# Kernel optimization log

Hardware: AMD Instinct MI355X
Metric: run time of the kernel (lower is better)

Reference implementation:

```python
import jax, jax.numpy as jnp
import numpy as np
from jax import lax

K_NN = 20          # cfg.nsample
BN_EPS = 1e-5


def fps(xyz, npoint, farthest0):
    """Furthest point sampling. xyz: [B,N,3] -> idx [B,npoint] (int)."""
    B, N, _ = xyz.shape

    def step(carry, _):
        distance, far = carry                                  # [B,N], [B]
        centroid = jnp.take_along_axis(xyz, far[:, None, None], axis=1)  # [B,1,3]
        d = jnp.sum((xyz - centroid) ** 2, axis=-1)            # [B,N]
        distance = jnp.minimum(distance, d)
        new_far = jnp.argmax(distance, axis=-1)
        return (distance, new_far), far

    init = (jnp.full((B, N), 1e10, dtype=xyz.dtype), farthest0)
    (_, _), idxs = lax.scan(step, init, None, length=npoint)   # idxs: [npoint,B]
    return jnp.transpose(idxs)                                 # [B,npoint]


def setup_inputs() -> dict:
    key = jax.random.key(0)
    k1, k2, k3, k4 = jax.random.split(key, 4)
    B, N, C = 4, 8192, 128
    c_in = C * 2 + 6   # mlps[0]*2 + 6 (use_xyz) = 262
    c_out = 256
    xyz = jax.random.normal(k1, (B, N, 3), dtype=jnp.float32)
    feat = jax.random.normal(k2, (B, N, C), dtype=jnp.float32)
    conv_w = jax.random.normal(k3, (c_in, c_out), dtype=jnp.float32) * 0.05  # 1x1 conv
    bn_gamma = jnp.ones((c_out,), dtype=jnp.float32)
    bn_beta = jnp.zeros((c_out,), dtype=jnp.float32)
    init_farthest = jax.random.randint(k4, (B,), 0, N)
    return {"xyz": xyz, "feat": feat, "conv_w": conv_w, "bn_gamma": bn_gamma,
            "bn_beta": bn_beta, "init_farthest": init_farthest, "npoints": 2048}


def reference(xyz, feat, conv_w, bn_gamma, bn_beta, init_farthest, npoints):
    # --- FPS sampling ---
    sample_idx = fps(xyz, npoints, init_farthest)                      # [B,S]
    new_xyz = jnp.take_along_axis(xyz, sample_idx[:, :, None], axis=1)  # [B,S,3]

    # --- augment features with xyz (use_xyz=True) ---
    feat_aug = jnp.concatenate([feat, xyz], axis=-1)                   # [B,N,131]
    new_feat_aug = jnp.take_along_axis(feat_aug, sample_idx[:, :, None], axis=1)  # [B,S,131]

    # --- KNN of new_xyz in xyz (squared L2, ascending) ---
    d2 = (jnp.sum(new_xyz ** 2, -1)[:, :, None]
          - 2.0 * jnp.einsum('bsd,bnd->bsn', new_xyz, xyz)
          + jnp.sum(xyz ** 2, -1)[:, None, :])                         # [B,S,N]
    _, knn_idx = lax.top_k(-d2, K_NN)                                  # [B,S,K]

    # --- gather neighbor features, build edge features ---
    knn_feat = jax.vmap(lambda f, i: f[i])(feat_aug, knn_idx)          # [B,S,K,131]
    center = new_feat_aug[:, :, None, :]                               # [B,S,1,131]
    edge = jnp.concatenate(
        [knn_feat - center, jnp.broadcast_to(center, knn_feat.shape)], axis=-1)  # [B,S,K,262]

    # --- shared MLP: 1x1 conv + BN (batch stats) + ReLU ---
    h = jnp.einsum('bskc,co->bsko', edge, conv_w)                      # [B,S,K,256]
    mean = jnp.mean(h, axis=(0, 1, 2))
    var = jnp.var(h, axis=(0, 1, 2))
    h = (h - mean) * lax.rsqrt(var + BN_EPS) * bn_gamma + bn_beta
    h = jax.nn.relu(h)

    # --- max-pool over K neighbors ---
    new_feat = jnp.max(h, axis=2)                                      # [B,S,256]
    return (new_xyz, new_feat, sample_idx)
```

## Files before the change

### kernel.cpp

```cpp
#include <hip/hip_runtime.h>
#include <hip/hip_bf16.h>


#define NPTS   8192
#define NSAMP  2048
#define KNN    20

typedef unsigned long long u64;
typedef unsigned int u32;
typedef unsigned short u16;

template<int CTRL, int RM>
__device__ __forceinline__ u64 dpp_kmax(u64 k) {
  unsigned lo = (unsigned)k, hi = (unsigned)(k >> 32);
  unsigned lo2 = (unsigned)__builtin_amdgcn_update_dpp((int)lo, (int)lo, CTRL, RM, 0xf, false);
  unsigned hi2 = (unsigned)__builtin_amdgcn_update_dpp((int)hi, (int)hi, CTRL, RM, 0xf, false);
  u64 o = ((u64)hi2 << 32) | lo2;
  return o > k ? o : k;
}
template<int CTRL, int RM>
__device__ __forceinline__ u64 dpp_kmin(u64 k) {
  unsigned lo = (unsigned)k, hi = (unsigned)(k >> 32);
  unsigned lo2 = (unsigned)__builtin_amdgcn_update_dpp((int)lo, (int)lo, CTRL, RM, 0xf, false);
  unsigned hi2 = (unsigned)__builtin_amdgcn_update_dpp((int)hi, (int)hi, CTRL, RM, 0xf, false);
  u64 o = ((u64)hi2 << 32) | lo2;
  return o < k ? o : k;
}
__device__ __forceinline__ u64 umax64(u64 a, u64 b) { return a > b ? a : b; }

__device__ __forceinline__ unsigned mspread4(unsigned q) {
  return (q & 1u) | ((q & 2u) << 2) | ((q & 4u) << 4) | ((q & 8u) << 6);
}

__global__ __launch_bounds__(1024, 1) void fps_kernel(
    const float* __restrict__ xyz, const int* __restrict__ farthest0,
    int* __restrict__ sample_int, float* __restrict__ out) {
  __shared__ float sxs[NPTS], sys[NPTS], szs[NPTS];
  __shared__ u16   sidxr[NPTS];
  __shared__ u32   s_samp[NSAMP];
  __shared__ u32   hist[4096];
  __shared__ u32   part[1024];
  __shared__ u64   slot[3];
  __shared__ int   s_isp;
  const int b = blockIdx.x, tid = threadIdx.x, lane = tid & 63;
  const float* xb = xyz + (size_t)b * NPTS * 3;

  for (int i = tid; i < 4096; i += 1024) hist[i] = 0u;
  if (tid < 3) slot[tid] = 0ull;
  __syncthreads();

  float ox[8], oy[8], oz[8];
  int cell[8];
#pragma unroll
  for (int j = 0; j < 8; ++j) {
    int p = tid * 8 + j;
    float x = xb[3*p], y = xb[3*p+1], z = xb[3*p+2];
    ox[j] = x; oy[j] = y; oz[j] = z;
    unsigned qx = (unsigned)(int)fminf(fmaxf((x + 5.2f) * 1.5384615f, 0.f), 15.f);
    unsigned qy = (unsigned)(int)fminf(fmaxf((y + 5.2f) * 1.5384615f, 0.f), 15.f);
    unsigned qz = (unsigned)(int)fminf(fmaxf((z + 5.2f) * 1.5384615f, 0.f), 15.f);
    cell[j] = (int)(mspread4(qx) | (mspread4(qy) << 1) | (mspread4(qz) << 2));
    atomicAdd(&hist[cell[j]], 1u);
  }
  __syncthreads();

  u32 h0 = hist[4*tid], h1 = hist[4*tid+1], h2 = hist[4*tid+2], h3 = hist[4*tid+3];
  u32 mysum = h0 + h1 + h2 + h3;
  part[tid] = mysum;
  __syncthreads();
  for (int off = 1; off < 1024; off <<= 1) {
    u32 u = (tid >= off) ? part[tid - off] : 0u;
    u32 v = part[tid];
    __syncthreads();
    part[tid] = u + v;
    __syncthreads();
  }
  u32 base = part[tid] - mysum;
  hist[4*tid]   = base;
  hist[4*tid+1] = base + h0;
  hist[4*tid+2] = base + h0 + h1;
  hist[4*tid+3] = base + h0 + h1 + h2;
  __syncthreads();

#pragma unroll
  for (int j = 0; j < 8; ++j) {
    u32 p = atomicAdd(&hist[cell[j]], 1u);
    sxs[p] = ox[j]; sys[p] = oy[j]; szs[p] = oz[j];
    sidxr[p] = (u16)(tid * 8 + j);
  }
  __syncthreads();

  const int cur0 = farthest0[b];
#pragma unroll
  for (int j = 0; j < 8; ++j) {
    int p = tid * 8 + j;
    if ((int)sidxr[p] == cur0) s_isp = p;
  }

  float px[8], py[8], pz[8], dist[8];
  u32 low26[8];
#pragma unroll
  for (int j = 0; j < 8; ++j) {
    int p = tid * 8 + j;
    px[j] = sxs[p]; py[j] = sys[p]; pz[j] = szs[p];
    low26[j] = (((~(u32)sidxr[p]) & 0x1FFFu) << 13) | (u32)p;
    dist[j] = 1e10f;
  }
  float lxmin = px[0], lxmax = px[0], lymin = py[0], lymax = py[0], lzmin = pz[0], lzmax = pz[0];
#pragma unroll
  for (int j = 1; j < 8; ++j) {
    lxmin = fminf(lxmin, px[j]); lxmax = fmaxf(lxmax, px[j]);
    lymin = fminf(lymin, py[j]); lymax = fmaxf(lymax, py[j]);
    lzmin = fminf(lzmin, pz[j]); lzmax = fmaxf(lzmax, pz[j]);
  }

  u64 klane = ((u64)__float_as_uint(1e10f) << 26);
  u64 kw    = ((u64)__float_as_uint(1e10f) << 26);
  __syncthreads();

  int cur_sp = s_isp;
  u32 cur_pack = ((u32)cur0 << 13) | (u32)cur_sp;

  for (int it = 0; it < NSAMP; ++it) {
    if (tid == 0) s_samp[it] = cur_pack;
    if (it == NSAMP - 1) break;
    if (tid == 64) slot[(it+2)%3] = 0ull;
    float cx = sxs[cur_sp], cy = sys[cur_sp], cz = szs[cur_sp];

    float gx = fmaxf(fmaxf(__fsub_rn(lxmin, cx), __fsub_rn(cx, lxmax)), 0.f);
    float gy = fmaxf(fmaxf(__fsub_rn(lymin, cy), __fsub_rn(cy, lymax)), 0.f);
    float gz = fmaxf(fmaxf(__fsub_rn(lzmin, cz), __fsub_rn(cz, lzmax)), 0.f);
    float bound = __fadd_rn(__fadd_rn(__fmul_rn(gx,gx), __fmul_rn(gy,gy)), __fmul_rn(gz,gz));
    float ub = __uint_as_float((u32)(klane >> 26));
    bool live = !(__fmul_rn(bound, 0.999999f) >= ub);

    if (__any(live)) {
      if (live) {
#pragma unroll
        for (int j = 0; j < 8; ++j) {
          float dx = __fsub_rn(px[j], cx);
          float dy = __fsub_rn(py[j], cy);
          float dz = __fsub_rn(pz[j], cz);
          float d  = __fadd_rn(__fadd_rn(__fmul_rn(dx,dx), __fmul_rn(dy,dy)), __fmul_rn(dz,dz));
          dist[j] = fminf(dist[j], d);
        }
        u64 k0 = ((u64)__float_as_uint(dist[0]) << 26) | low26[0];
        u64 k1 = ((u64)__float_as_uint(dist[1]) << 26) | low26[1];
        u64 k2 = ((u64)__float_as_uint(dist[2]) << 26) | low26[2];
        u64 k3 = ((u64)__float_as_uint(dist[3]) << 26) | low26[3];
        u64 k4 = ((u64)__float_as_uint(dist[4]) << 26) | low26[4];
        u64 k5 = ((u64)__float_as_uint(dist[5]) << 26) | low26[5];
        u64 k6 = ((u64)__float_as_uint(dist[6]) << 26) | low26[6];
        u64 k7 = ((u64)__float_as_uint(dist[7]) << 26) | low26[7];
        klane = umax64(umax64(umax64(k0,k1), umax64(k2,k3)),
                       umax64(umax64(k4,k5), umax64(k6,k7)));
      }
      u64 k = klane;
      k = dpp_kmax<0xB1, 0xf>(k);
      k = dpp_kmax<0x4E, 0xf>(k);
      k = dpp_kmax<0x124, 0xf>(k);
      k = dpp_kmax<0x128, 0xf>(k);
      k = dpp_kmax<0x142, 0xa>(k);
      k = dpp_kmax<0x143, 0xc>(k);
      kw = k;
    }
    if (lane == 63) atomicMax(&slot[(it+1)%3], kw);
    __syncthreads();
    u64 wk = slot[(it+1)%3];
    cur_sp = (int)(wk & 0x1FFFu);
    u32 org = (~(u32)(wk >> 13)) & 0x1FFFu;
    cur_pack = (org << 13) | (u32)cur_sp;
  }

  __syncthreads();
  float* outxyz = out + (size_t)b * NSAMP * 3;
  float* outidx = out + 24576 + 2097152 + (size_t)b * NSAMP;
  for (int it = tid; it < NSAMP; it += 1024) {
    u32 s = s_samp[it];
    int org = (int)(s >> 13), sp = (int)(s & 0x1FFFu);
    sample_int[(b << 11) + it] = org;
    outidx[it] = (float)org;
    outxyz[3*it]   = sxs[sp];
    outxyz[3*it+1] = sys[sp];
    outxyz[3*it+2] = szs[sp];
  }
}

__global__ __launch_bounds__(256, 1) void knn_kernel(
    const float* __restrict__ xyz, const int* __restrict__ sample_int,
    int* __restrict__ knn_out) {
  __shared__ u64 lists[2][2][KNN];
  const int tid  = threadIdx.x;
  const int lane = tid & 63, w = tid >> 6;
  const int ql   = w >> 1;
  const int ch   = w & 1;
  const int qq   = blockIdx.x * 2 + ql;
  const int b    = qq >> 11;
  const float* xb = xyz + (size_t)b * NPTS * 3;
  const int sidx = sample_int[qq];
  const float sx = xb[3*sidx], sy = xb[3*sidx+1], sz = xb[3*sidx+2];
  const float sqs = __fadd_rn(__fadd_rn(__fmul_rn(sx,sx), __fmul_rn(sy,sy)), __fmul_rn(sz,sz));

  const int pbase = ch * 4096;
  float d[64];
#pragma unroll
  for (int i = 0; i < 64; ++i) {
    int p = pbase + i*64 + lane;
    float x = xb[3*p], y = xb[3*p+1], z = xb[3*p+2];
    float dot = __fadd_rn(__fadd_rn(__fmul_rn(sx,x), __fmul_rn(sy,y)), __fmul_rn(sz,z));
    float sqx = __fadd_rn(__fadd_rn(__fmul_rn(x,x), __fmul_rn(y,y)), __fmul_rn(z,z));
    d[i] = __fadd_rn(__fsub_rn(sqs, __fmul_rn(2.0f, dot)), sqx);
  }
  u64 msk = 0ull;
  for (int kk = 0; kk < KNN; ++kk) {
    float bv = 1e30f; int bs = 0;
#pragma unroll
    for (int i = 0; i < 64; ++i) {
      float dc = (msk & (1ull << i)) ? 1e30f : d[i];
      if (dc < bv) { bv = dc; bs = i; }
    }
    unsigned gi = (unsigned)(pbase + bs*64 + lane);
    u64 key = ((u64)__float_as_uint(bv) << 32) | gi;
    key = dpp_kmin<0xB1, 0xf>(key);
    key = dpp_kmin<0x4E, 0xf>(key);
    key = dpp_kmin<0x124, 0xf>(key);
    key = dpp_kmin<0x128, 0xf>(key);
    key = dpp_kmin<0x142, 0xa>(key);
    key = dpp_kmin<0x143, 0xc>(key);
    unsigned glo = (unsigned)__builtin_amdgcn_readlane((int)(unsigned)key, 63);
    unsigned ghi = (unsigned)__builtin_amdgcn_readlane((int)(unsigned)(key >> 32), 63);
    if (lane == (int)(glo & 63u)) msk |= 1ull << ((glo - pbase) >> 6);
    if (lane == 0) lists[ql][ch][kk] = ((u64)ghi << 32) | glo;
  }
  __syncthreads();
  if (ch == 0) {
    u64 mykey = ~0ull; int rank = 64;
    if (lane < 40) {
      int li = lane >= 20 ? 1 : 0;
      int e  = li ? lane - 20 : lane;
      mykey = lists[ql][li][e];
      int cnt = e;
      const u64* oth = &lists[ql][li ^ 1][0];
#pragma unroll
      for (int j = 0; j < KNN; ++j) cnt += (oth[j] < mykey) ? 1 : 0;
      rank = cnt;
    }
    if (rank < KNN) knn_out[(size_t)qq * KNN + rank] = (int)(mykey & 0xFFFFFFFFull);
  }
}

__global__ void wdiff_kernel(const float* __restrict__ W, float* __restrict__ Wd) {
  int i = blockIdx.x * 256 + threadIdx.x;
  Wd[i] = W[131*256 + i] - W[i];
}

template<bool BF16OUT>
__global__ __launch_bounds__(128) void matmul131_kernel(
    const float* __restrict__ featb, const float* __restrict__ xyzb,
    const int* __restrict__ gidx,
    const float* __restrict__ W, void* __restrict__ outp) {
  __shared__ float tile[32][132];
  const int tid = threadIdx.x;
  const int r0  = blockIdx.x << 5;
  for (int i = tid; i < 32*131; i += 128) {
    int r = i / 131;
    int k = i - r*131;
    int row = r0 + r;
    int src;
    if (gidx) { int bb = row >> 11; src = (bb << 13) + gidx[row]; }
    else      { src = row; }
    float v = (k < 128) ? featb[(size_t)src*128 + k]
                        : xyzb[(size_t)src*3 + (k-128)];
    tile[r][k] = v;
  }
  __syncthreads();
  float acc0[32], acc1[32];
#pragma unroll
  for (int r = 0; r < 32; ++r) { acc0[r] = 0.f; acc1[r] = 0.f; }
  const int c0 = tid, c1 = tid + 128;
  for (int k = 0; k < 128; k += 4) {
    float w00 = W[(k+0)*256+c0], w01 = W[(k+1)*256+c0], w02 = W[(k+2)*256+c0], w03 = W[(k+3)*256+c0];
    float w10 = W[(k+0)*256+c1], w11 = W[(k+1)*256+c1], w12 = W[(k+2)*256+c1], w13 = W[(k+3)*256+c1];
#pragma unroll
    for (int r = 0; r < 32; ++r) {
      float4 a = *(const float4*)&tile[r][k];
      acc0[r] = fmaf(a.x, w00, acc0[r]); acc0[r] = fmaf(a.y, w01, acc0[r]);
      acc0[r] = fmaf(a.z, w02, acc0[r]); acc0[r] = fmaf(a.w, w03, acc0[r]);
      acc1[r] = fmaf(a.x, w10, acc1[r]); acc1[r] = fmaf(a.y, w11, acc1[r]);
      acc1[r] = fmaf(a.z, w12, acc1[r]); acc1[r] = fmaf(a.w, w13, acc1[r]);
    }
  }
#pragma unroll
  for (int kk = 128; kk < 131; ++kk) {
    float w0 = W[kk*256+c0], w1 = W[kk*256+c1];
#pragma unroll
    for (int r = 0; r < 32; ++r) {
      float a = tile[r][kk];
      acc0[r] = fmaf(a, w0, acc0[r]);
      acc1[r] = fmaf(a, w1, acc1[r]);
    }
  }
#pragma unroll
  for (int r = 0; r < 32; ++r) {
    if (BF16OUT) {
      __hip_bfloat16* o = (__hip_bfloat16*)outp;
      o[(size_t)(r0+r)*256 + c0] = __float2bfloat16(acc0[r]);
      o[(size_t)(r0+r)*256 + c1] = __float2bfloat16(acc1[r]);
    } else {
      float* o = (float*)outp;
      o[(size_t)(r0+r)*256 + c0] = acc0[r];
      o[(size_t)(r0+r)*256 + c1] = acc1[r];
    }
  }
}

__global__ __launch_bounds__(256) void stats_kernel(
    const __hip_bfloat16* __restrict__ Pb,
    const int* __restrict__ knn, float* __restrict__ outFeat,
    float* __restrict__ psum, float* __restrict__ psq, int qq0, int prow) {
  const int c = threadIdx.x;
  float s = 0.f, s2 = 0.f;
  const int q0 = qq0 + blockIdx.x * 16;
  for (int q = 0; q < 16; ++q) {
    int qq = q0 + q;
    float qc = outFeat[(size_t)qq*256 + c];
    float m = -1e30f;
    const int* kn = knn + (size_t)qq * KNN;
#pragma unroll
    for (int k = 0; k < KNN; ++k) {
      int idx = kn[k];
      float v = __bfloat162float(Pb[(size_t)idx*256 + c]) + qc;
      m = fmaxf(m, v);
      s += v;
      s2 = fmaf(v, v, s2);
    }
    outFeat[(size_t)qq*256 + c] = m;
  }
  psum[(size_t)(prow + blockIdx.x)*256 + c] = s;
  psq [(size_t)(prow + blockIdx.x)*256 + c] = s2;
}

__global__ __launch_bounds__(256) void reduce_stats_kernel(
    const float* __restrict__ psum, const float* __restrict__ psq,
    const float* __restrict__ gamma, const float* __restrict__ beta,
    float* __restrict__ ss) {
  const int c = blockIdx.x, t = threadIdx.x;
  float s  = psum[(size_t)t*256 + c] + psum[(size_t)(t+256)*256 + c];
  float s2 = psq [(size_t)t*256 + c] + psq [(size_t)(t+256)*256 + c];
#pragma unroll
  for (int off = 32; off >= 1; off >>= 1) {
    s  += __shfl_xor(s,  off);
    s2 += __shfl_xor(s2, off);
  }
  __shared__ float as[4], as2[4];
  const int lane = t & 63, wid = t >> 6;
  if (lane == 0) { as[wid] = s; as2[wid] = s2; }
  __syncthreads();
  if (t == 0) {
    float S  = (as[0]+as[1]) + (as[2]+as[3]);
    float S2 = (as2[0]+as2[1]) + (as2[2]+as2[3]);
    const float inv = 1.f / 163840.f;
    float mean = S * inv;
    float var  = S2 * inv - mean * mean;
    float sc = rsqrtf(var + 1e-5f) * gamma[c];
    ss[c]       = sc;
    ss[256 + c] = beta[c] - mean * sc;
  }
}

__global__ __launch_bounds__(256) void finalize_kernel(
    float* __restrict__ f, const float* __restrict__ ss) {
  int e = blockIdx.x * 256 + threadIdx.x;
  float v = fmaf(f[e], ss[threadIdx.x], ss[256 + threadIdx.x]);
  f[e] = v > 0.f ? v : 0.f;
}

extern "C" void kernel_launch(void* const* d_in, const int* in_sizes, int n_in,
                              void* d_out, int out_size, void* d_ws, size_t ws_size,
                              hipStream_t stream) {
  const float* xyz      = (const float*)d_in[0];
  const float* feat     = (const float*)d_in[1];
  const float* conv_w   = (const float*)d_in[2];
  const float* bn_gamma = (const float*)d_in[3];
  const float* bn_beta  = (const float*)d_in[4];
  const int*   far0     = (const int*)d_in[5];

  char* ws = (char*)d_ws;
  int*   sample_int = (int*)  (ws + 0);
  int*   knn        = (int*)  (ws + 32768);
  float* Wd         = (float*)(ws + 688128);
  float* psum       = (float*)(ws + 822272);
  float* psq        = (float*)(ws + 1346560);
  float* ss         = (float*)(ws + 1870848);
  __hip_bfloat16* Pb = (__hip_bfloat16*)(ws + 2097152);

  float* out     = (float*)d_out;
  float* outFeat = out + 24576;

  fps_kernel  <<<dim3(4),    dim3(1024), 0, stream>>>(xyz, far0, sample_int, out);
  knn_kernel  <<<dim3(4096), dim3(256),  0, stream>>>(xyz, sample_int, knn);
  wdiff_kernel<<<dim3(131),  dim3(256),  0, stream>>>(conv_w, Wd);

  matmul131_kernel<false><<<dim3(256), dim3(128), 0, stream>>>(
      feat, xyz, sample_int, Wd, (void*)outFeat);

  for (int b = 0; b < 4; ++b) {
    matmul131_kernel<true><<<dim3(256), dim3(128), 0, stream>>>(
        feat + (size_t)b*NPTS*128, xyz + (size_t)b*NPTS*3,
        (const int*)nullptr, conv_w, (void*)Pb);
    stats_kernel<<<dim3(128), dim3(256), 0, stream>>>(
        Pb, knn + (size_t)b*NSAMP*KNN, outFeat + (size_t)b*NSAMP*256,
        psum, psq, 0, b*128);
  }

  reduce_stats_kernel<<<dim3(256), dim3(256), 0, stream>>>(psum, psq, bn_gamma, bn_beta, ss);
  finalize_kernel   <<<dim3(8192), dim3(256), 0, stream>>>(outFeat, ss);
}
```

Before: 2.242 ms.

## Batch all four matmul+stats passes into single launches and repack FPS shared layout

When the workspace is large enough, the per-batch loop of four matmul and four stats launches becomes one larger matmul grid over all batches and one stats kernel that picks the batch per query. This fills the GPU better and removes launch gaps, at the cost of a bigger bf16 intermediate buffer. FPS also moves to an interleaved xyz shared array with a float3 centroid load. The argmax key packing changes to a 32-bit shift so the winning index can be read from the low word.

```diff
diff --git a/kernel.cpp b/kernel.cpp
--- a/kernel.cpp
+++ b/kernel.cpp
@@ -35,7 +35,7 @@
 __global__ __launch_bounds__(1024, 1) void fps_kernel(
     const float* __restrict__ xyz, const int* __restrict__ farthest0,
     int* __restrict__ sample_int, float* __restrict__ out) {
-  __shared__ float sxs[NPTS], sys[NPTS], szs[NPTS];
+  __shared__ float sxyz[NPTS * 3];
   __shared__ u16   sidxr[NPTS];
   __shared__ u32   s_samp[NSAMP];
   __shared__ u32   hist[4096];
@@ -85,7 +85,7 @@
 #pragma unroll
   for (int j = 0; j < 8; ++j) {
     u32 p = atomicAdd(&hist[cell[j]], 1u);
-    sxs[p] = ox[j]; sys[p] = oy[j]; szs[p] = oz[j];
+    sxyz[3*p] = ox[j]; sxyz[3*p+1] = oy[j]; sxyz[3*p+2] = oz[j];
     sidxr[p] = (u16)(tid * 8 + j);
   }
   __syncthreads();
@@ -98,12 +98,12 @@
   }
 
   float px[8], py[8], pz[8], dist[8];
-  u32 low26[8];
+  u32 low32[8];
 #pragma unroll
   for (int j = 0; j < 8; ++j) {
     int p = tid * 8 + j;
-    px[j] = sxs[p]; py[j] = sys[p]; pz[j] = szs[p];
-    low26[j] = (((~(u32)sidxr[p]) & 0x1FFFu) << 13) | (u32)p;
+    px[j] = sxyz[3*p]; py[j] = sxyz[3*p+1]; pz[j] = sxyz[3*p+2];
+    low32[j] = (((~(u32)sidxr[p]) & 0x1FFFu) << 13) | (u32)p;
     dist[j] = 1e10f;
   }
   float lxmin = px[0], lxmax = px[0], lymin = py[0], lymax = py[0], lzmin = pz[0], lzmax = pz[0];
@@ -114,8 +114,8 @@
     lzmin = fminf(lzmin, pz[j]); lzmax = fmaxf(lzmax, pz[j]);
   }
 
-  u64 klane = ((u64)__float_as_uint(1e10f) << 26);
-  u64 kw    = ((u64)__float_as_uint(1e10f) << 26);
+  u64 klane = ((u64)__float_as_uint(1e10f) << 32);
+  u64 kw    = ((u64)__float_as_uint(1e10f) << 32);
   __syncthreads();
 
   int cur_sp = s_isp;
@@ -125,13 +125,14 @@
     if (tid == 0) s_samp[it] = cur_pack;
     if (it == NSAMP - 1) break;
     if (tid == 64) slot[(it+2)%3] = 0ull;
-    float cx = sxs[cur_sp], cy = sys[cur_sp], cz = szs[cur_sp];
+    float3 c3 = *(const float3*)&sxyz[3*cur_sp];
+    float cx = c3.x, cy = c3.y, cz = c3.z;
 
     float gx = fmaxf(fmaxf(__fsub_rn(lxmin, cx), __fsub_rn(cx, lxmax)), 0.f);
     float gy = fmaxf(fmaxf(__fsub_rn(lymin, cy), __fsub_rn(cy, lymax)), 0.f);
     float gz = fmaxf(fmaxf(__fsub_rn(lzmin, cz), __fsub_rn(cz, lzmax)), 0.f);
     float bound = __fadd_rn(__fadd_rn(__fmul_rn(gx,gx), __fmul_rn(gy,gy)), __fmul_rn(gz,gz));
-    float ub = __uint_as_float((u32)(klane >> 26));
+    float ub = __uint_as_float((u32)(klane >> 32));
     bool live = !(__fmul_rn(bound, 0.999999f) >= ub);
 
     if (__any(live)) {
@@ -144,14 +145,14 @@
           float d  = __fadd_rn(__fadd_rn(__fmul_rn(dx,dx), __fmul_rn(dy,dy)), __fmul_rn(dz,dz));
           dist[j] = fminf(dist[j], d);
         }
-        u64 k0 = ((u64)__float_as_uint(dist[0]) << 26) | low26[0];
-        u64 k1 = ((u64)__float_as_uint(dist[1]) << 26) | low26[1];
-        u64 k2 = ((u64)__float_as_uint(dist[2]) << 26) | low26[2];
-        u64 k3 = ((u64)__float_as_uint(dist[3]) << 26) | low26[3];
-        u64 k4 = ((u64)__float_as_uint(dist[4]) << 26) | low26[4];
-        u64 k5 = ((u64)__float_as_uint(dist[5]) << 26) | low26[5];
-        u64 k6 = ((u64)__float_as_uint(dist[6]) << 26) | low26[6];
-        u64 k7 = ((u64)__float_as_uint(dist[7]) << 26) | low26[7];
+        u64 k0 = ((u64)__float_as_uint(dist[0]) << 32) | low32[0];
+        u64 k1 = ((u64)__float_as_uint(dist[1]) << 32) | low32[1];
+        u64 k2 = ((u64)__float_as_uint(dist[2]) << 32) | low32[2];
+        u64 k3 = ((u64)__float_as_uint(dist[3]) << 32) | low32[3];
+        u64 k4 = ((u64)__float_as_uint(dist[4]) << 32) | low32[4];
+        u64 k5 = ((u64)__float_as_uint(dist[5]) << 32) | low32[5];
+        u64 k6 = ((u64)__float_as_uint(dist[6]) << 32) | low32[6];
+        u64 k7 = ((u64)__float_as_uint(dist[7]) << 32) | low32[7];
         klane = umax64(umax64(umax64(k0,k1), umax64(k2,k3)),
                        umax64(umax64(k4,k5), umax64(k6,k7)));
       }
@@ -167,8 +168,9 @@
     if (lane == 63) atomicMax(&slot[(it+1)%3], kw);
     __syncthreads();
     u64 wk = slot[(it+1)%3];
-    cur_sp = (int)(wk & 0x1FFFu);
-    u32 org = (~(u32)(wk >> 13)) & 0x1FFFu;
+    u32 wlo = (u32)wk;
+    cur_sp = (int)(wlo & 0x1FFFu);
+    u32 org = (~(wlo >> 13)) & 0x1FFFu;
     cur_pack = (org << 13) | (u32)cur_sp;
   }
 
@@ -180,9 +182,9 @@
     int org = (int)(s >> 13), sp = (int)(s & 0x1FFFu);
     sample_int[(b << 11) + it] = org;
     outidx[it] = (float)org;
-    outxyz[3*it]   = sxs[sp];
-    outxyz[3*it+1] = sys[sp];
-    outxyz[3*it+2] = szs[sp];
+    outxyz[3*it]   = sxyz[3*sp];
+    outxyz[3*it+1] = sxyz[3*sp+1];
+    outxyz[3*it+2] = sxyz[3*sp+2];
   }
 }
 
@@ -315,9 +317,9 @@
 }
 
 __global__ __launch_bounds__(256) void stats_kernel(
-    const __hip_bfloat16* __restrict__ Pb,
-    const int* __restrict__ knn, float* __restrict__ outFeat,
-    float* __restrict__ psum, float* __restrict__ psq, int qq0, int prow) {
+    const __hip_bfloat16* __restrict__ Pb, const int* __restrict__ knn,
+    float* __restrict__ outFeat, float* __restrict__ psum, float* __restrict__ psq,
+    int qq0, int prow) {
   const int c = threadIdx.x;
   float s = 0.f, s2 = 0.f;
   const int q0 = qq0 + blockIdx.x * 16;
@@ -338,6 +340,34 @@
   }
   psum[(size_t)(prow + blockIdx.x)*256 + c] = s;
   psq [(size_t)(prow + blockIdx.x)*256 + c] = s2;
+}
+
+__global__ __launch_bounds__(256) void stats_all_kernel(
+    const __hip_bfloat16* __restrict__ Pall,
+    const int* __restrict__ knn, float* __restrict__ outFeat,
+    float* __restrict__ psum, float* __restrict__ psq) {
+  const int c = threadIdx.x;
+  float s = 0.f, s2 = 0.f;
+  const int q0 = blockIdx.x * 16;
+  for (int q = 0; q < 16; ++q) {
+    int qq = q0 + q;
+    int b = qq >> 11;
+    const __hip_bfloat16* Pb = Pall + (size_t)b * NPTS * 256;
+    float qc = outFeat[(size_t)qq*256 + c];
+    float m = -1e30f;
+    const int* kn = knn + (size_t)qq * KNN;
+#pragma unroll
+    for (int k = 0; k < KNN; ++k) {
+      int idx = kn[k];
+      float v = __bfloat162float(Pb[(size_t)idx*256 + c]) + qc;
+      m = fmaxf(m, v);
+      s += v;
+      s2 = fmaf(v, v, s2);
+    }
+    outFeat[(size_t)qq*256 + c] = m;
+  }
+  psum[(size_t)blockIdx.x*256 + c] = s;
+  psq [(size_t)blockIdx.x*256 + c] = s2;
 }
 
 __global__ __launch_bounds__(256) void reduce_stats_kernel(
@@ -397,6 +427,8 @@
   float* out     = (float*)d_out;
   float* outFeat = out + 24576;
 
+  const bool fused = ws_size >= (size_t)(2097152 + 33554432/2);
+
   fps_kernel  <<<dim3(4),    dim3(1024), 0, stream>>>(xyz, far0, sample_int, out);
   knn_kernel  <<<dim3(4096), dim3(256),  0, stream>>>(xyz, sample_int, knn);
   wdiff_kernel<<<dim3(131),  dim3(256),  0, stream>>>(conv_w, Wd);
@@ -404,13 +436,20 @@
   matmul131_kernel<false><<<dim3(256), dim3(128), 0, stream>>>(
       feat, xyz, sample_int, Wd, (void*)outFeat);
 
-  for (int b = 0; b < 4; ++b) {
-    matmul131_kernel<true><<<dim3(256), dim3(128), 0, stream>>>(
-        feat + (size_t)b*NPTS*128, xyz + (size_t)b*NPTS*3,
-        (const int*)nullptr, conv_w, (void*)Pb);
-    stats_kernel<<<dim3(128), dim3(256), 0, stream>>>(
-        Pb, knn + (size_t)b*NSAMP*KNN, outFeat + (size_t)b*NSAMP*256,
-        psum, psq, 0, b*128);
+  if (fused) {
+    matmul131_kernel<true><<<dim3(1024), dim3(128), 0, stream>>>(
+        feat, xyz, (const int*)nullptr, conv_w, (void*)Pb);
+    stats_all_kernel<<<dim3(512), dim3(256), 0, stream>>>(
+        Pb, knn, outFeat, psum, psq);
+  } else {
+    for (int b = 0; b < 4; ++b) {
+      matmul131_kernel<true><<<dim3(256), dim3(128), 0, stream>>>(
+          feat + (size_t)b*NPTS*128, xyz + (size_t)b*NPTS*3,
+          (const int*)nullptr, conv_w, (void*)Pb);
+      stats_kernel<<<dim3(128), dim3(256), 0, stream>>>(
+          Pb, knn + (size_t)b*NSAMP*KNN, outFeat + (size_t)b*NSAMP*256,
+          psum, psq, 0, b*128);
+    }
   }
 
   reduce_stats_kernel<<<dim3(256), dim3(256), 0, stream>>>(psum, psq, bn_gamma, bn_beta, ss);
```

New measurement: 1.918 ms. 14.4% less time.
